# Optimization experiments

Measured on AMD Instinct MI355X. Metric: run time of the kernel, lower is better.

Reference implementation:

```python
import jax, jax.numpy as jnp
import numpy as np

B, S, H, V = 64, 256, 1024, 10000


def setup_inputs() -> dict:
    key = jax.random.key(0)
    ks = jax.random.split(key, 16)
    s = 1.0 / np.sqrt(H)
    return {
        "input_seq": jax.random.randint(ks[0], (B,), 0, V),
        "last_hidden": jax.random.normal(ks[1], (1, 1, H), jnp.float32),
        "encoder_outputs": jax.random.normal(ks[2], (S, B, H), jnp.float32),
        "emb_table": jax.random.normal(ks[3], (V, H), jnp.float32) * s,
        "W_ih": jax.random.normal(ks[4], (3 * H, H), jnp.float32) * s,
        "W_hh": jax.random.normal(ks[5], (3 * H, H), jnp.float32) * s,
        "b_ih": jax.random.normal(ks[6], (3 * H,), jnp.float32) * s,
        "b_hh": jax.random.normal(ks[7], (3 * H,), jnp.float32) * s,
        "W_attn": jax.random.normal(ks[8], (H, 2 * H), jnp.float32) * s,
        "b_attn": jax.random.normal(ks[9], (H,), jnp.float32) * s,
        "v_attn": jax.random.normal(ks[10], (H,), jnp.float32) * s,
        "W_concat": jax.random.normal(ks[11], (H, 2 * H), jnp.float32) * s,
        "b_concat": jax.random.normal(ks[12], (H,), jnp.float32) * s,
        "W_out": jax.random.normal(ks[13], (V, H), jnp.float32) * s,
        "b_out": jax.random.normal(ks[14], (V,), jnp.float32) * s,
    }


def _gru_scan(x_seq, h0, W_ih, W_hh, b_ih, b_hh):
    # x_seq: [T, H] (here T == batch dim, per the module's batch_first quirk)
    def step(h, x):
        gi = x @ W_ih.T + b_ih   # [3H]
        gh = h @ W_hh.T + b_hh   # [3H]
        ir, iz, inn = jnp.split(gi, 3)
        hr, hz, hn = jnp.split(gh, 3)
        r = jax.nn.sigmoid(ir + hr)
        z = jax.nn.sigmoid(iz + hz)
        n = jnp.tanh(inn + r * hn)
        h_new = (1.0 - z) * n + z * h
        return h_new, h_new

    h_last, outs = jax.lax.scan(step, h0, x_seq)
    return outs, h_last


def reference(input_seq, last_hidden, encoder_outputs, emb_table, W_ih, W_hh,
              b_ih, b_hh, W_attn, b_attn, v_attn, W_concat, b_concat, W_out, b_out):
    embedded = emb_table[input_seq]                       # [B, H]
    # GRU fed [1, B, H] with batch_first=True -> recurs over B with one hidden
    rnn_output, h_last = _gru_scan(embedded, last_hidden[0, 0], W_ih, W_hh, b_ih, b_hh)
    hidden = h_last[None, None, :]                        # [1, 1, H]

    # concat attention: score(b,i) = v . (W_attn @ [h_b ; enc_ib] + b_attn)
    enc = jnp.transpose(encoder_outputs, (1, 0, 2))       # [B, S, H]
    h_bc = jnp.broadcast_to(rnn_output[:, None, :], (B, S, H))
    cat = jnp.concatenate([h_bc, enc], axis=-1)           # [B, S, 2H]
    energy = jnp.einsum('bsk,hk->bsh', cat, W_attn) + b_attn
    scores = jnp.einsum('bsh,h->bs', energy, v_attn)      # [B, S]
    attn_weights = jax.nn.softmax(scores, axis=-1)[:, None, :]  # [B, 1, S]

    context = jnp.einsum('bs,bsh->bh', attn_weights[:, 0, :], enc)  # [B, H]
    concat_input = jnp.concatenate([rnn_output, context], axis=-1)  # [B, 2H]
    concat_output = jnp.tanh(concat_input @ W_concat.T + b_concat)  # [B, H]
    output = concat_output @ W_out.T + b_out                        # [B, V]
    return output, hidden, attn_weights
```

## Files before the change

kernel.cpp:

```cpp
#include <hip/hip_runtime.h>
#include <math.h>

#define kH  1024
#define kB  64
#define kS  256
#define kV  10000
#define kH3 3072

__device__ __forceinline__ float warp_sum(float v) {
#pragma unroll
  for (int off = 32; off > 0; off >>= 1) v += __shfl_down(v, off, 64);
  return v;
}
__device__ __forceinline__ float warp_max_all(float v) {
#pragma unroll
  for (int off = 32; off > 0; off >>= 1) v = fmaxf(v, __shfl_xor(v, off, 64));
  return v;
}
__device__ __forceinline__ float warp_sum_all(float v) {
#pragma unroll
  for (int off = 32; off > 0; off >>= 1) v += __shfl_xor(v, off, 64);
  return v;
}
__device__ __forceinline__ float sigmoidf_(float x) { return 1.0f / (1.0f + __expf(-x)); }

__global__ __launch_bounds__(256) void k_gi(const int* __restrict__ seq,
    const float* __restrict__ emb, const float* __restrict__ W_ih,
    const float* __restrict__ b_ih, float* __restrict__ GI) {
  const int lane = threadIdx.x & 63;
  const int r = blockIdx.x * 4 + (threadIdx.x >> 6);
  const float4* wp = (const float4*)(W_ih + (size_t)r * kH) + lane * 4;
  const float4 w0 = wp[0], w1 = wp[1], w2 = wp[2], w3 = wp[3];
  const float br = b_ih[r];
  for (int t = 0; t < kB; ++t) {
    const int tok = seq[t];
    const float4* xp = (const float4*)(emb + (size_t)tok * kH) + lane * 4;
    const float4 x0 = xp[0], x1 = xp[1], x2 = xp[2], x3 = xp[3];
    float acc = w0.x*x0.x + w0.y*x0.y + w0.z*x0.z + w0.w*x0.w;
    acc += w1.x*x1.x + w1.y*x1.y + w1.z*x1.z + w1.w*x1.w;
    acc += w2.x*x2.x + w2.y*x2.y + w2.z*x2.z + w2.w*x2.w;
    acc += w3.x*x3.x + w3.y*x3.y + w3.z*x3.z + w3.w*x3.w;
    acc = warp_sum(acc);
    if (lane == 0) GI[(size_t)t * kH3 + r] = acc + br;
  }
}

__global__ __launch_bounds__(512, 2) void k_gru(const float* __restrict__ h0,
    const float* __restrict__ W_hh, const float* __restrict__ b_hh,
    const float* __restrict__ GI, float* __restrict__ rnn,
    unsigned long long* __restrict__ step) {
  __shared__ float hs[2][kH];
  const int tid  = threadIdx.x;
  const int lane = tid & 63;
  const int w    = tid >> 6;
  const int bid  = blockIdx.x;
  const int j    = bid * 16 + 2 * w;

  float wv[6][16];
  {
    const int rows[6] = { j, j + 1, kH + j, kH + j + 1, 2 * kH + j, 2 * kH + j + 1 };
#pragma unroll
    for (int q = 0; q < 6; ++q) {
      const float* base = W_hh + (size_t)rows[q] * kH + lane;
#pragma unroll
      for (int u = 0; u < 16; ++u) wv[q][u] = base[u * 64];
    }
  }
  const float2 bhr = *(const float2*)(b_hh + j);
  const float2 bhz = *(const float2*)(b_hh + kH + j);
  const float2 bhn = *(const float2*)(b_hh + 2 * kH + j);

  for (int t = 0; t < kB; ++t) {
    float2 gir = *(const float2*)(GI + (size_t)t * kH3 + j);
    float2 giz = *(const float2*)(GI + (size_t)t * kH3 + kH + j);
    float2 gin = *(const float2*)(GI + (size_t)t * kH3 + 2 * kH + j);
    asm volatile("" :: "v"(gir.x), "v"(gir.y), "v"(giz.x), "v"(giz.y),
                       "v"(gin.x), "v"(gin.y));

    float* hb = hs[t & 1];
    if (t == 0) {
      ((float2*)hb)[tid] = ((const float2*)h0)[tid];
    } else {
      const unsigned long long* sb = step + (size_t)(t - 1) * kH;
      const int i0 = tid * 2, i1 = i0 + 1;
      const unsigned want = (unsigned)t;
      bool d0 = false, d1 = false;
      float v0 = 0.f, v1 = 0.f;
      while (true) {
        if (!d0) {
          const unsigned long long x = __hip_atomic_load(&sb[i0],
              __ATOMIC_RELAXED, __HIP_MEMORY_SCOPE_AGENT);
          if ((unsigned)(x >> 32) == want) { v0 = __uint_as_float((unsigned)x); d0 = true; }
        }
        if (!d1) {
          const unsigned long long x = __hip_atomic_load(&sb[i1],
              __ATOMIC_RELAXED, __HIP_MEMORY_SCOPE_AGENT);
          if ((unsigned)(x >> 32) == want) { v1 = __uint_as_float((unsigned)x); d1 = true; }
        }
        if (d0 && d1) break;
        __builtin_amdgcn_s_sleep(1);
      }
      hb[i0] = v0; hb[i1] = v1;
    }
    __syncthreads();

    float hx[16];
#pragma unroll
    for (int u = 0; u < 16; ++u) hx[u] = hb[u * 64 + lane];

    float d[6];
#pragma unroll
    for (int q = 0; q < 6; ++q) {
      float acc = 0.f;
#pragma unroll
      for (int u = 0; u < 16; ++u) acc += wv[q][u] * hx[u];
      d[q] = acc;
    }
#pragma unroll
    for (int q = 0; q < 6; ++q) d[q] = warp_sum(d[q]);

    if (lane == 0) {
      const float ho0 = hb[j], ho1 = hb[j + 1];
      const float r0 = sigmoidf_(gir.x + d[0] + bhr.x);
      const float r1 = sigmoidf_(gir.y + d[1] + bhr.y);
      const float z0 = sigmoidf_(giz.x + d[2] + bhz.x);
      const float z1 = sigmoidf_(giz.y + d[3] + bhz.y);
      const float n0 = tanhf(gin.x + r0 * (d[4] + bhn.x));
      const float n1 = tanhf(gin.y + r1 * (d[5] + bhn.y));
      float2 hn;
      hn.x = (1.f - z0) * n0 + z0 * ho0;
      hn.y = (1.f - z1) * n1 + z1 * ho1;
      *(float2*)(rnn + (size_t)t * kH + j) = hn;
      const unsigned long long tagw = ((unsigned long long)(t + 1)) << 32;
      __hip_atomic_store(&step[(size_t)t * kH + j], tagw | __float_as_uint(hn.x),
                         __ATOMIC_RELAXED, __HIP_MEMORY_SCOPE_AGENT);
      __hip_atomic_store(&step[(size_t)t * kH + j + 1], tagw | __float_as_uint(hn.y),
                         __ATOMIC_RELAXED, __HIP_MEMORY_SCOPE_AGENT);
    }
  }
}

__global__ __launch_bounds__(256) void k_w2h(const float* __restrict__ W_attn,
    const float* __restrict__ v_attn, float* __restrict__ w2h) {
  __shared__ float4 red[256];
  const int t  = threadIdx.x;
  const int k0 = kH + blockIdx.x * 4;
  float ax = 0, ay = 0, az = 0, aw = 0;
  for (int h = t; h < kH; h += 256) {
    const float vh = v_attn[h];
    const float4 wq = *(const float4*)(W_attn + (size_t)h * 2048 + k0);
    ax += vh * wq.x; ay += vh * wq.y; az += vh * wq.z; aw += vh * wq.w;
  }
  red[t] = make_float4(ax, ay, az, aw);
  __syncthreads();
  for (int s = 128; s > 0; s >>= 1) {
    if (t < s) {
      const float4 a = red[t], b = red[t + s];
      red[t] = make_float4(a.x + b.x, a.y + b.y, a.z + b.z, a.w + b.w);
    }
    __syncthreads();
  }
  if (t == 0) *(float4*)(w2h + blockIdx.x * 4) = red[0];
}

__global__ __launch_bounds__(256) void k_scores(const float* __restrict__ enc,
    const float* __restrict__ w2h, float* __restrict__ sc) {
  const int lane = threadIdx.x & 63;
  const int wg = blockIdx.x * 4 + (threadIdx.x >> 6);
  const int b = wg & 63, s = wg >> 6;
  const float4* ep = (const float4*)(enc + ((size_t)s * kB + b) * kH) + lane * 4;
  const float4* wp = (const float4*)w2h + lane * 4;
  float acc = 0.f;
#pragma unroll
  for (int c = 0; c < 4; ++c) {
    const float4 e = ep[c], wq = wp[c];
    acc += e.x * wq.x + e.y * wq.y + e.z * wq.z + e.w * wq.w;
  }
  acc = warp_sum(acc);
  if (lane == 0) sc[b * kS + s] = acc;
}

__global__ __launch_bounds__(256) void k_softmax(const float* __restrict__ sc,
                                                 float* __restrict__ attn) {
  __shared__ float sm[4], ss[4];
  const int b = blockIdx.x, t = threadIdx.x, lane = t & 63, w = t >> 6;
  const float x = sc[b * kS + t];
  float m = warp_max_all(x);
  if (lane == 0) sm[w] = m;
  __syncthreads();
  m = fmaxf(fmaxf(sm[0], sm[1]), fmaxf(sm[2], sm[3]));
  const float e = __expf(x - m);
  float s = warp_sum_all(e);
  if (lane == 0) ss[w] = s;
  __syncthreads();
  s = ss[0] + ss[1] + ss[2] + ss[3];
  attn[b * kS + t] = e / s;
}

__global__ __launch_bounds__(256) void k_context(const float* __restrict__ enc,
    const float* __restrict__ attn, float* __restrict__ part) {
  const int b  = blockIdx.x & 63;
  const int ch = blockIdx.x >> 6;
  const int h0 = threadIdx.x * 4;
  float ax = 0, ay = 0, az = 0, aw = 0;
  const int s0 = ch * 64;
  for (int s = s0; s < s0 + 64; ++s) {
    const float a = attn[b * kS + s];
    const float4 v = *(const float4*)(enc + ((size_t)s * kB + b) * kH + h0);
    ax += a * v.x; ay += a * v.y; az += a * v.z; aw += a * v.w;
  }
  *(float4*)(part + ((size_t)ch * kB + b) * kH + h0) =
      make_float4(ax, ay, az, aw);
}

__global__ __launch_bounds__(256) void k_ctxsum(const float* __restrict__ part,
    const float* __restrict__ rnn, float* __restrict__ ctx,
    float* __restrict__ hid) {
  const int b = blockIdx.x;
  const int h0 = threadIdx.x * 4;
  float4 s = *(const float4*)(part + ((size_t)0 * kB + b) * kH + h0);
#pragma unroll
  for (int c = 1; c < 4; ++c) {
    const float4 p = *(const float4*)(part + ((size_t)c * kB + b) * kH + h0);
    s.x += p.x; s.y += p.y; s.z += p.z; s.w += p.w;
  }
  *(float4*)(ctx + (size_t)b * kH + h0) = s;
  if (b < 4) {
    const int i = b * 256 + threadIdx.x;
    hid[i] = rnn[63 * kH + i];
  }
}

__global__ __launch_bounds__(256) void k_concat(const float* __restrict__ rnn,
    const float* __restrict__ ctx, const float* __restrict__ W_c,
    const float* __restrict__ b_c, float* __restrict__ coT) {
  const int lane = threadIdx.x & 63;
  const int i = blockIdx.x * 4 + (threadIdx.x >> 6);
  float wreg[32];
  {
    const float4* wp = (const float4*)(W_c + (size_t)i * 2048) + lane * 8;
#pragma unroll
    for (int c = 0; c < 8; ++c) {
      const float4 f = wp[c];
      wreg[c * 4 + 0] = f.x; wreg[c * 4 + 1] = f.y;
      wreg[c * 4 + 2] = f.z; wreg[c * 4 + 3] = f.w;
    }
  }
  const float bc = b_c[i];
  const int jcol = lane * 32;
  const float* xbase = (jcol < kH) ? (rnn + jcol) : (ctx + (jcol - kH));
  for (int b = 0; b < kB; ++b) {
    const float* xr = xbase + (size_t)b * kH;
    float acc = 0.f;
#pragma unroll
    for (int c = 0; c < 8; ++c) {
      const float4 x = *(const float4*)(xr + c * 4);
      acc += wreg[c * 4 + 0] * x.x + wreg[c * 4 + 1] * x.y +
             wreg[c * 4 + 2] * x.z + wreg[c * 4 + 3] * x.w;
    }
    acc = warp_sum(acc);
    if (lane == 0) coT[(size_t)i * kB + b] = tanhf(acc + bc);
  }
}

__global__ __launch_bounds__(256) void k_out(const float* __restrict__ coT,
    const float* __restrict__ W_out, const float* __restrict__ b_out,
    float* __restrict__ out) {
  const int lane = threadIdx.x & 63;
  int wg = blockIdx.x * 4 + (threadIdx.x >> 6);
  wg = __builtin_amdgcn_readfirstlane(wg);
  const int v0 = wg * 10;
  float acc[10];
#pragma unroll
  for (int i = 0; i < 10; ++i) acc[i] = 0.f;
  for (int h = 0; h < kH; h += 4) {
    const float x0 = coT[(h + 0) * kB + lane];
    const float x1 = coT[(h + 1) * kB + lane];
    const float x2 = coT[(h + 2) * kB + lane];
    const float x3 = coT[(h + 3) * kB + lane];
#pragma unroll
    for (int i = 0; i < 10; ++i) {
      const float4 wq = *(const float4*)(W_out + (size_t)(v0 + i) * kH + h);
      acc[i] += wq.x * x0 + wq.y * x1 + wq.z * x2 + wq.w * x3;
    }
  }
#pragma unroll
  for (int i = 0; i < 10; ++i)
    out[(size_t)lane * kV + v0 + i] = acc[i] + b_out[v0 + i];
}

extern "C" void kernel_launch(void* const* d_in, const int* in_sizes, int n_in,
                              void* d_out, int out_size, void* d_ws,
                              size_t ws_size, hipStream_t stream) {
  const int*   seq    = (const int*)  d_in[0];
  const float* h0     = (const float*)d_in[1];
  const float* enc    = (const float*)d_in[2];
  const float* emb    = (const float*)d_in[3];
  const float* W_ih   = (const float*)d_in[4];
  const float* W_hh   = (const float*)d_in[5];
  const float* b_ih   = (const float*)d_in[6];
  const float* b_hh   = (const float*)d_in[7];
  const float* W_attn = (const float*)d_in[8];
  const float* v_attn = (const float*)d_in[10];
  const float* W_conc = (const float*)d_in[11];
  const float* b_conc = (const float*)d_in[12];
  const float* W_outp = (const float*)d_in[13];
  const float* b_outp = (const float*)d_in[14];

  float* out      = (float*)d_out;
  float* out_hid  = out + 640000;
  float* out_attn = out + 641024;

  float* ws = (float*)d_ws;
  float* GI   = ws;
  float* RNN  = ws + 196608;
  unsigned long long* STEP =
      (unsigned long long*)(ws + 262144);
  float* W2H  = ws + 393216;
  float* SC   = ws + 394240;
  float* PART = ws + 410624;
  float* CTX  = ws + 672768;
  float* COT  = ws + 738304;

  k_gi<<<768, 256, 0, stream>>>(seq, emb, W_ih, b_ih, GI);
  k_gru<<<64, 512, 0, stream>>>(h0, W_hh, b_hh, GI, RNN, STEP);
  k_w2h<<<256, 256, 0, stream>>>(W_attn, v_attn, W2H);
  k_scores<<<4096, 256, 0, stream>>>(enc, W2H, SC);
  k_softmax<<<64, 256, 0, stream>>>(SC, out_attn);
  k_context<<<256, 256, 0, stream>>>(enc, out_attn, PART);
  k_ctxsum<<<64, 256, 0, stream>>>(PART, RNN, CTX, out_hid);
  k_concat<<<256, 256, 0, stream>>>(RNN, CTX, W_conc, b_conc, COT);
  k_out<<<250, 256, 0, stream>>>(COT, W_outp, b_outp, out);
}
```

Baseline: 626.2 us.

## Stage W_out tiles in LDS, use fast gate math, pin GRU weights in registers

The output projection now copies a 16-row tile of W_out into shared memory per block and has each wave compute 4 vocab rows for 64 batch lanes with float4 stores. The grid grows from 250 to 625 blocks, trading the old per-lane broadcast global loads for LDS reads and more parallelism. The GRU step swaps tanhf and the sigmoid divide for fast exp/fdividef forms, which are slightly less accurate. It also adds empty asm barriers to keep W_hh in registers, and partially unrolls the context loop.

```diff
diff --git a/kernel.cpp b/kernel.cpp
--- a/kernel.cpp
+++ b/kernel.cpp
@@ -22,7 +22,14 @@
   for (int off = 32; off > 0; off >>= 1) v += __shfl_xor(v, off, 64);
   return v;
 }
-__device__ __forceinline__ float sigmoidf_(float x) { return 1.0f / (1.0f + __expf(-x)); }
+__device__ __forceinline__ float sigmoidf_(float x) {
+  return __fdividef(1.0f, 1.0f + __expf(-x));
+}
+__device__ __forceinline__ float tanhf_(float x) {
+  const float t = __expf(-2.0f * fabsf(x));
+  const float r = __fdividef(1.0f - t, 1.0f + t);
+  return copysignf(r, x);
+}
 
 __global__ __launch_bounds__(256) void k_gi(const int* __restrict__ seq,
     const float* __restrict__ emb, const float* __restrict__ W_ih,
@@ -66,6 +73,12 @@
       for (int u = 0; u < 16; ++u) wv[q][u] = base[u * 64];
     }
   }
+#pragma unroll
+  for (int q = 0; q < 6; ++q)
+#pragma unroll
+    for (int u = 0; u < 16; ++u)
+      asm volatile("" : "+v"(wv[q][u]));
+
   const float2 bhr = *(const float2*)(b_hh + j);
   const float2 bhz = *(const float2*)(b_hh + kH + j);
   const float2 bhn = *(const float2*)(b_hh + 2 * kH + j);
@@ -125,8 +138,8 @@
       const float r1 = sigmoidf_(gir.y + d[1] + bhr.y);
       const float z0 = sigmoidf_(giz.x + d[2] + bhz.x);
       const float z1 = sigmoidf_(giz.y + d[3] + bhz.y);
-      const float n0 = tanhf(gin.x + r0 * (d[4] + bhn.x));
-      const float n1 = tanhf(gin.y + r1 * (d[5] + bhn.y));
+      const float n0 = tanhf_(gin.x + r0 * (d[4] + bhn.x));
+      const float n1 = tanhf_(gin.y + r1 * (d[5] + bhn.y));
       float2 hn;
       hn.x = (1.f - z0) * n0 + z0 * ho0;
       hn.y = (1.f - z1) * n1 + z1 * ho1;
@@ -204,6 +217,7 @@
   const int h0 = threadIdx.x * 4;
   float ax = 0, ay = 0, az = 0, aw = 0;
   const int s0 = ch * 64;
+#pragma unroll 4
   for (int s = s0; s < s0 + 64; ++s) {
     const float a = attn[b * kS + s];
     const float4 v = *(const float4*)(enc + ((size_t)s * kB + b) * kH + h0);
@@ -266,27 +280,39 @@
 __global__ __launch_bounds__(256) void k_out(const float* __restrict__ coT,
     const float* __restrict__ W_out, const float* __restrict__ b_out,
     float* __restrict__ out) {
+  __shared__ float wlds[16 * kH];
+  const int v0 = blockIdx.x * 16;
+  {
+    const float4* src = (const float4*)(W_out + (size_t)v0 * kH);
+    float4 tmp[16];
+#pragma unroll
+    for (int c = 0; c < 16; ++c) tmp[c] = src[threadIdx.x + 256 * c];
+    float4* dst = (float4*)wlds;
+#pragma unroll
+    for (int c = 0; c < 16; ++c) dst[threadIdx.x + 256 * c] = tmp[c];
+  }
+  __syncthreads();
+
   const int lane = threadIdx.x & 63;
-  int wg = blockIdx.x * 4 + (threadIdx.x >> 6);
-  wg = __builtin_amdgcn_readfirstlane(wg);
-  const int v0 = wg * 10;
-  float acc[10];
-#pragma unroll
-  for (int i = 0; i < 10; ++i) acc[i] = 0.f;
+  const int w    = threadIdx.x >> 6;
+  float acc[4] = {0.f, 0.f, 0.f, 0.f};
+#pragma unroll 2
   for (int h = 0; h < kH; h += 4) {
-    const float x0 = coT[(h + 0) * kB + lane];
-    const float x1 = coT[(h + 1) * kB + lane];
-    const float x2 = coT[(h + 2) * kB + lane];
-    const float x3 = coT[(h + 3) * kB + lane];
-#pragma unroll
-    for (int i = 0; i < 10; ++i) {
-      const float4 wq = *(const float4*)(W_out + (size_t)(v0 + i) * kH + h);
-      acc[i] += wq.x * x0 + wq.y * x1 + wq.z * x2 + wq.w * x3;
-    }
-  }
-#pragma unroll
-  for (int i = 0; i < 10; ++i)
-    out[(size_t)lane * kV + v0 + i] = acc[i] + b_out[v0 + i];
+    const float x0 = coT[(size_t)(h + 0) * kB + lane];
+    const float x1 = coT[(size_t)(h + 1) * kB + lane];
+    const float x2 = coT[(size_t)(h + 2) * kB + lane];
+    const float x3 = coT[(size_t)(h + 3) * kB + lane];
+#pragma unroll
+    for (int vi = 0; vi < 4; ++vi) {
+      const float4 wq = *(const float4*)&wlds[(w * 4 + vi) * kH + h];
+      acc[vi] += wq.x * x0 + wq.y * x1 + wq.z * x2 + wq.w * x3;
+    }
+  }
+  const float4 bq = *(const float4*)(b_out + v0 + w * 4);
+  float4 r;
+  r.x = acc[0] + bq.x; r.y = acc[1] + bq.y;
+  r.z = acc[2] + bq.z; r.w = acc[3] + bq.w;
+  *(float4*)&out[(size_t)lane * kV + v0 + w * 4] = r;
 }
 
 extern "C" void kernel_launch(void* const* d_in, const int* in_sizes, int n_in,
@@ -330,5 +356,5 @@
   k_context<<<256, 256, 0, stream>>>(enc, out_attn, PART);
   k_ctxsum<<<64, 256, 0, stream>>>(PART, RNN, CTX, out_hid);
   k_concat<<<256, 256, 0, stream>>>(RNN, CTX, W_conc, b_conc, COT);
-  k_out<<<250, 256, 0, stream>>>(COT, W_outp, b_outp, out);
-}
+  k_out<<<625, 256, 0, stream>>>(COT, W_outp, b_outp, out);
+}
```

Result: no change. 638.3 us (+1.9%).
